# Kernel tuning notes

Measured on AMD Instinct MI355X. Metric: run time of the kernel, lower is better.

Reference implementation:

```python
import jax, jax.numpy as jnp
import numpy as np

EPS = 1e-5  # torch LayerNorm default

def _ln(x, w, b):
    mu = jnp.mean(x, axis=-1, keepdims=True)
    var = jnp.mean((x - mu) ** 2, axis=-1, keepdims=True)
    return (x - mu) * jax.lax.rsqrt(var + EPS) * w + b

def setup_inputs() -> dict:
    B, C, P, D = 256, 256, 256, 256  # broadcasting in final add requires B==P==C
    key = jax.random.key(0)
    ks = jax.random.split(key, 10)
    d_rsqrt = D ** -0.5
    return {
        "x": jax.random.normal(ks[0], (B, C), dtype=jnp.float32),
        "prev_cell_out": jax.random.normal(ks[1], (P, D), dtype=jnp.float32),
        "feature_emb_weight": jax.random.uniform(ks[2], (C, D), minval=-d_rsqrt, maxval=d_rsqrt),
        "feature_emb_bias": jax.random.uniform(ks[3], (1, C, D), minval=-d_rsqrt, maxval=d_rsqrt),
        "ln_emb_w": jnp.ones((D,), jnp.float32), "ln_emb_b": jnp.zeros((D,), jnp.float32),
        "ln_col_w": jnp.ones((D,), jnp.float32), "ln_col_b": jnp.zeros((D,), jnp.float32),
        "ln_prompt_w": jnp.ones((D,), jnp.float32), "ln_prompt_b": jnp.zeros((D,), jnp.float32),
        "dense_imp_w": jax.random.normal(ks[4], (D, 2 * D)) * (2 * D) ** -0.5,  # torch Linear weight [out,in]
        "dense_imp_b": jnp.zeros((D,), jnp.float32),
        "emb_column": jax.random.normal(ks[5], (C, D)) * 0.01,
        "emb_prompt": jax.random.normal(ks[6], (P, D)) * 0.01,
        "expand_weight": jax.random.normal(ks[7], (P, 1)),  # dense_expand.weight [n_prompts, 1]
        "expand_bias": jax.random.normal(ks[8], (P,)) * 0.01,
    }

def reference(x, prev_cell_out, feature_emb_weight, feature_emb_bias,
              ln_emb_w, ln_emb_b, ln_col_w, ln_col_b, ln_prompt_w, ln_prompt_b,
              dense_imp_w, dense_imp_b, emb_column, emb_prompt,
              expand_weight, expand_bias):
    # addcmul: bias + x[...,None] * weight -> [B, C, D]
    x_emb = _ln(jax.nn.relu(feature_emb_bias + x[..., None] * feature_emb_weight), ln_emb_w, ln_emb_b)
    # prompt path (unbatched): [P, 2D] -> [P, D]
    xp_in = jnp.concatenate([_ln(emb_prompt, ln_prompt_w, ln_prompt_b), prev_cell_out], axis=-1)
    x_prompt = xp_in @ dense_imp_w.T + dense_imp_b + emb_prompt
    x_col = _ln(emb_column, ln_col_w, ln_col_b)  # [C, D]
    mask = jax.nn.softmax(x_prompt @ x_col.T, axis=-1)  # [P, C]
    # einsum 'pc,bcd->bpd'
    x_out = jnp.einsum('pc,bcd->bpd', mask, x_emb)
    # 'pc,bcd,pa->bpd' with a==1 is the same contraction scaled per-prompt by expand_weight[p,0]
    x_out = x_out * (1.0 + expand_weight[:, 0])[None, :, None]
    # 'pc,p->pc' then unsqueeze(0).unsqueeze(-1): [1, P, C, 1]; broadcasts [B,P,D] -> [1,B,P,D]
    bias_term = (mask * expand_bias[:, None])[None, :, :, None]
    return x_out + bias_term  # [1, B, P, D] (B==P==C)
```

## Files before the change

### kernel.cpp

```cpp
#include <hip/hip_runtime.h>
#include <cstdint>

typedef _Float16 half8 __attribute__((ext_vector_type(8)));
typedef float f32x4 __attribute__((ext_vector_type(4)));

#define LN_EPS 1e-5f

__device__ __forceinline__ float dot4(float4 a, float4 b) {
  return a.x*b.x + a.y*b.y + a.z*b.z + a.w*b.w;
}

__global__ __launch_bounds__(256) void k_pre(
    const float* __restrict__ x, const float* __restrict__ few, const float* __restrict__ feb,
    const float* __restrict__ emb_pr, const float* __restrict__ lnp_w, const float* __restrict__ lnp_b,
    const float* __restrict__ prev, const float* __restrict__ W, const float* __restrict__ Wb,
    const float* __restrict__ emb_col, const float* __restrict__ lnc_w, const float* __restrict__ lnc_b,
    float2* __restrict__ stats2, float* __restrict__ mask_f32, _Float16* __restrict__ mask_f16)
{
  __shared__ __align__(16) struct {
    float xin[512];
    float xq[256];
    float sc[256];
    float wr1[4], wr2[4];
  } sm;

  int t = threadIdx.x, w = t >> 6, lane = t & 63;

  if (blockIdx.x >= 256) {
    int bid = blockIdx.x - 256;
    int b = bid >> 3;
    int cg = (bid & 7) * 4 + w;
    int c0 = cg * 8;
    float xv[8];
    #pragma unroll
    for (int j = 0; j < 8; ++j) xv[j] = x[b*256 + c0 + j];
    float s1[8], s2[8];
    #pragma unroll
    for (int j = 0; j < 8; ++j) { s1[j] = 0.f; s2[j] = 0.f; }
    #pragma unroll
    for (int j = 0; j < 8; ++j) {
      float4 fw = ((const float4*)few)[(c0+j)*64 + lane];
      float4 fb = ((const float4*)feb)[(c0+j)*64 + lane];
      float4 v;
      v.x = fmaxf(fb.x + xv[j]*fw.x, 0.f);
      v.y = fmaxf(fb.y + xv[j]*fw.y, 0.f);
      v.z = fmaxf(fb.z + xv[j]*fw.z, 0.f);
      v.w = fmaxf(fb.w + xv[j]*fw.w, 0.f);
      s1[j] += v.x + v.y + v.z + v.w;
      s2[j] += v.x*v.x + v.y*v.y + v.z*v.z + v.w*v.w;
    }
    #pragma unroll
    for (int o = 32; o > 0; o >>= 1) {
      #pragma unroll
      for (int j = 0; j < 8; ++j) { s1[j] += __shfl_xor(s1[j], o); s2[j] += __shfl_xor(s2[j], o); }
    }
    float mu[8], rs[8];
    #pragma unroll
    for (int j = 0; j < 8; ++j) {
      mu[j] = s1[j] * (1.0f/256.0f);
      float var = s2[j] * (1.0f/256.0f) - mu[j]*mu[j];
      rs[j] = rsqrtf(var + LN_EPS);
    }
    float muv = mu[0], rsv = rs[0];
    #pragma unroll
    for (int j = 1; j < 8; ++j) {
      muv = (lane == j) ? mu[j] : muv;
      rsv = (lane == j) ? rs[j] : rsv;
    }
    if (lane < 8) stats2[b*256 + c0 + lane] = make_float2(muv, rsv);
    return;
  }

  int p = blockIdx.x;
  int q = t & 3, g = t >> 2;

  {
    float4 v = ((const float4*)emb_pr)[p*64 + lane];
    float s1 = v.x + v.y + v.z + v.w;
    float s2 = v.x*v.x + v.y*v.y + v.z*v.z + v.w*v.w;
    #pragma unroll
    for (int o = 32; o > 0; o >>= 1) { s1 += __shfl_xor(s1, o); s2 += __shfl_xor(s2, o); }
    float mu = s1 * (1.0f/256.0f);
    float var = s2 * (1.0f/256.0f) - mu*mu;
    float rsv = rsqrtf(var + LN_EPS);
    float4 w4 = ((const float4*)lnp_w)[lane];
    float4 b4 = ((const float4*)lnp_b)[lane];
    float4 y;
    y.x = (v.x-mu)*rsv*w4.x + b4.x;  y.y = (v.y-mu)*rsv*w4.y + b4.y;
    y.z = (v.z-mu)*rsv*w4.z + b4.z;  y.w = (v.w-mu)*rsv*w4.w + b4.w;
    if (w == 0) {
      ((float4*)sm.xin)[lane] = y;
      ((float4*)sm.xin)[64 + lane] = ((const float4*)prev)[p*64 + lane];
    }
  }
  __syncthreads();

  {
    float acc[4] = {0.f, 0.f, 0.f, 0.f};
    #pragma unroll 4
    for (int j = 0; j < 32; ++j) {
      int k4 = j*4 + q;
      float4 xv = ((const float4*)sm.xin)[k4];
      #pragma unroll
      for (int pp = 0; pp < 4; ++pp) {
        int d = pp*64 + g;
        float4 wv = ((const float4*)W)[d*128 + k4];
        acc[pp] += dot4(wv, xv);
      }
    }
    #pragma unroll
    for (int pp = 0; pp < 4; ++pp) {
      acc[pp] += __shfl_xor(acc[pp], 1);
      acc[pp] += __shfl_xor(acc[pp], 2);
    }
    if (q == 0) {
      #pragma unroll
      for (int pp = 0; pp < 4; ++pp) {
        int d = pp*64 + g;
        sm.xq[d] = acc[pp] + Wb[d] + emb_pr[p*256 + d];
      }
    }
  }
  __syncthreads();

  {
    float s1[4] = {0,0,0,0}, s2[4] = {0,0,0,0};
    #pragma unroll 4
    for (int j = 0; j < 16; ++j) {
      int k4 = j*4 + q;
      #pragma unroll
      for (int pp = 0; pp < 4; ++pp) {
        float4 v = ((const float4*)emb_col)[(pp*64+g)*64 + k4];
        s1[pp] += v.x + v.y + v.z + v.w;
        s2[pp] += v.x*v.x + v.y*v.y + v.z*v.z + v.w*v.w;
      }
    }
    float mu[4], rs[4];
    #pragma unroll
    for (int pp = 0; pp < 4; ++pp) {
      s1[pp] += __shfl_xor(s1[pp], 1);  s1[pp] += __shfl_xor(s1[pp], 2);
      s2[pp] += __shfl_xor(s2[pp], 1);  s2[pp] += __shfl_xor(s2[pp], 2);
      mu[pp] = s1[pp] * (1.0f/256.0f);
      float var = s2[pp] * (1.0f/256.0f) - mu[pp]*mu[pp];
      rs[pp] = rsqrtf(var + LN_EPS);
    }
    float acc[4] = {0.f, 0.f, 0.f, 0.f};
    #pragma unroll 4
    for (int j = 0; j < 16; ++j) {
      int k4 = j*4 + q;
      float4 lw4 = ((const float4*)lnc_w)[k4];
      float4 lb4 = ((const float4*)lnc_b)[k4];
      float4 xv = ((const float4*)sm.xq)[k4];
      #pragma unroll
      for (int pp = 0; pp < 4; ++pp) {
        float4 v = ((const float4*)emb_col)[(pp*64+g)*64 + k4];
        float4 nc;
        nc.x = (v.x-mu[pp])*rs[pp]*lw4.x + lb4.x;
        nc.y = (v.y-mu[pp])*rs[pp]*lw4.y + lb4.y;
        nc.z = (v.z-mu[pp])*rs[pp]*lw4.z + lb4.z;
        nc.w = (v.w-mu[pp])*rs[pp]*lw4.w + lb4.w;
        acc[pp] += dot4(nc, xv);
      }
    }
    #pragma unroll
    for (int pp = 0; pp < 4; ++pp) {
      acc[pp] += __shfl_xor(acc[pp], 1);
      acc[pp] += __shfl_xor(acc[pp], 2);
    }
    if (q == 0) {
      #pragma unroll
      for (int pp = 0; pp < 4; ++pp) sm.sc[pp*64 + g] = acc[pp];
    }
  }
  __syncthreads();

  {
    float val = sm.sc[t];
    float m0 = val;
    #pragma unroll
    for (int o = 32; o > 0; o >>= 1) m0 = fmaxf(m0, __shfl_xor(m0, o));
    if (lane == 0) sm.wr1[w] = m0;
    __syncthreads();
    float M = fmaxf(fmaxf(sm.wr1[0], sm.wr1[1]), fmaxf(sm.wr1[2], sm.wr1[3]));
    float e = expf(val - M);
    float s = e;
    #pragma unroll
    for (int o = 32; o > 0; o >>= 1) s += __shfl_xor(s, o);
    if (lane == 0) sm.wr2[w] = s;
    __syncthreads();
    float S = sm.wr2[0] + sm.wr2[1] + sm.wr2[2] + sm.wr2[3];
    float mv = e / S;
    mask_f32[p*256 + t] = mv;
    mask_f16[p*256 + t] = (_Float16)mv;
  }
}

__global__ __launch_bounds__(256) void k_main(
    const float* __restrict__ x, const float* __restrict__ few, const float* __restrict__ feb,
    const float* __restrict__ ln_emb_w, const float* __restrict__ ln_emb_b,
    const float2* __restrict__ stats2,
    const _Float16* __restrict__ mask_f16, const float* __restrict__ mask_f32,
    const float* __restrict__ ew, const float* __restrict__ eb,
    float* __restrict__ out)
{
  __shared__ __align__(16) _Float16 Bs[2][8 * 64 * 8];
  __shared__ float xrow[256];
  __shared__ __align__(8) float2 srow[256];

  const int t = threadIdx.x, w = t >> 6, lane = t & 63;
  const int lm = lane & 15, quad = lane >> 4;
  const int b  = blockIdx.x >> 2;
  const int ds = (blockIdx.x & 3) * 64;
  const int dl = t & 63;
  const int d  = ds + dl;

  xrow[t] = x[b*256 + t];
  srow[t] = stats2[b*256 + t];
  const float lwv = ln_emb_w[d];
  const float lbv = ln_emb_b[d];

  f32x4 acc[4][4];
  #pragma unroll
  for (int i = 0; i < 4; ++i)
    #pragma unroll
    for (int j = 0; j < 4; ++j)
      acc[i][j] = (f32x4){0.f, 0.f, 0.f, 0.f};

  float fwv[16], fbv[16];
  #pragma unroll
  for (int j = 0; j < 16; ++j) {
    int cl = w*16 + j;
    fwv[j] = few[cl*256 + d];
    fbv[j] = feb[cl*256 + d];
  }
  __syncthreads();
  {
    half8 h0, h1;
    #pragma unroll
    for (int j = 0; j < 16; ++j) {
      int cl = w*16 + j;
      float2 st = srow[cl];
      float v = fmaxf(fbv[j] + xrow[cl]*fwv[j], 0.f);
      _Float16 hh = (_Float16)((v - st.x) * st.y * lwv + lbv);
      if (j < 8) h0[j] = hh; else h1[j-8] = hh;
    }
    *(half8*)(&Bs[0][((w*2 + 0)*64 + dl)*8]) = h0;
    *(half8*)(&Bs[0][((w*2 + 1)*64 + dl)*8]) = h1;
  }
  __syncthreads();

  for (int kb = 0; kb < 4; ++kb) {
    if (kb < 3) {
      #pragma unroll
      for (int j = 0; j < 16; ++j) {
        int cl = (kb+1)*64 + w*16 + j;
        fwv[j] = few[cl*256 + d];
        fbv[j] = feb[cl*256 + d];
      }
    }
    const _Float16* Bcur = &Bs[kb & 1][0];
    #pragma unroll
    for (int ks = 0; ks < 2; ++ks) {
      half8 af[4], bf[4];
      #pragma unroll
      for (int mt = 0; mt < 4; ++mt)
        af[mt] = *(const half8*)(mask_f16 + (size_t)(w*64 + mt*16 + lm)*256 + kb*64 + ks*32 + quad*8);
      #pragma unroll
      for (int nt = 0; nt < 4; ++nt)
        bf[nt] = *(const half8*)(Bcur + ((ks*4 + quad)*64 + nt*16 + lm)*8);
      #pragma unroll
      for (int mt = 0; mt < 4; ++mt)
        #pragma unroll
        for (int nt = 0; nt < 4; ++nt)
          acc[mt][nt] = __builtin_amdgcn_mfma_f32_16x16x32_f16(af[mt], bf[nt], acc[mt][nt], 0, 0, 0);
    }
    if (kb < 3) {
      half8 h0, h1;
      #pragma unroll
      for (int j = 0; j < 16; ++j) {
        int cl = (kb+1)*64 + w*16 + j;
        float2 st = srow[cl];
        float v = fmaxf(fbv[j] + xrow[cl]*fwv[j], 0.f);
        _Float16 hh = (_Float16)((v - st.x) * st.y * lwv + lbv);
        if (j < 8) h0[j] = hh; else h1[j-8] = hh;
      }
      *(half8*)(&Bs[(kb+1) & 1][((w*2 + 0)*64 + dl)*8]) = h0;
      *(half8*)(&Bs[(kb+1) & 1][((w*2 + 1)*64 + dl)*8]) = h1;
      __syncthreads();
    }
  }

  const float ebv = eb[b];
  #pragma unroll
  for (int mt = 0; mt < 4; ++mt) {
    float sp[4], tb[4];
    #pragma unroll
    for (int r = 0; r < 4; ++r) {
      int p = w*64 + mt*16 + quad*4 + r;
      sp[r] = 1.0f + ew[p];
      tb[r] = mask_f32[b*256 + p] * ebv;
    }
    #pragma unroll
    for (int nt = 0; nt < 4; ++nt) {
      int dd = ds + nt*16 + lm;
      #pragma unroll
      for (int r = 0; r < 4; ++r) {
        int p = w*64 + mt*16 + quad*4 + r;
        out[((size_t)b << 16) + ((size_t)p << 8) + dd] = acc[mt][nt][r] * sp[r] + tb[r];
      }
    }
  }
}

extern "C" void kernel_launch(void* const* d_in, const int* in_sizes, int n_in,
                              void* d_out, int out_size, void* d_ws, size_t ws_size,
                              hipStream_t stream) {
  const float* x        = (const float*)d_in[0];
  const float* prev     = (const float*)d_in[1];
  const float* few      = (const float*)d_in[2];
  const float* feb      = (const float*)d_in[3];
  const float* ln_emb_w = (const float*)d_in[4];
  const float* ln_emb_b = (const float*)d_in[5];
  const float* ln_col_w = (const float*)d_in[6];
  const float* ln_col_b = (const float*)d_in[7];
  const float* ln_pr_w  = (const float*)d_in[8];
  const float* ln_pr_b  = (const float*)d_in[9];
  const float* dimp_w   = (const float*)d_in[10];
  const float* dimp_b   = (const float*)d_in[11];
  const float* emb_col  = (const float*)d_in[12];
  const float* emb_pr   = (const float*)d_in[13];
  const float* ew       = (const float*)d_in[14];
  const float* eb       = (const float*)d_in[15];
  float* out = (float*)d_out;

  char* wsb = (char*)d_ws;
  float2*   ws_stats  = (float2*)(wsb);
  float*    ws_mask   = (float*)(wsb + 524288);
  _Float16* ws_mask_h = (_Float16*)(wsb + 786432);

  k_pre<<<dim3(256 + 2048), dim3(256), 0, stream>>>(
      x, few, feb,
      emb_pr, ln_pr_w, ln_pr_b, prev, dimp_w, dimp_b,
      emb_col, ln_col_w, ln_col_b,
      ws_stats, ws_mask, ws_mask_h);
  k_main<<<dim3(1024), dim3(256), 0, stream>>>(
      x, few, feb, ln_emb_w, ln_emb_b,
      ws_stats, ws_mask_h, ws_mask, ew, eb, out);
}
```

Measured before the change: 149.5 us.

## Swap MFMA operands for vectorized output stores and prefetch mask fragments

The MFMA operand roles are swapped so that the x_emb tile from LDS becomes the A operand and the mask the B operand. Each accumulator's four rows then run along d, so every lane writes its results with one 16-byte vector store instead of four scalar stores. Mask fragments for the next k-block are prefetched into registers during the current block's compute, and the kb loop is fully unrolled. This aims to cut store instruction count and hide global load latency, at the cost of higher register pressure.

```diff
diff --git a/kernel.cpp b/kernel.cpp
--- a/kernel.cpp
+++ b/kernel.cpp
@@ -214,6 +214,13 @@
   const int dl = t & 63;
   const int d  = ds + dl;
 
+  half8 mf[2][4];
+  #pragma unroll
+  for (int ks = 0; ks < 2; ++ks)
+    #pragma unroll
+    for (int nt = 0; nt < 4; ++nt)
+      mf[ks][nt] = *(const half8*)(mask_f16 + (size_t)(w*64 + nt*16 + lm)*256 + ks*32 + quad*8);
+
   xrow[t] = x[b*256 + t];
   srow[t] = stats2[b*256 + t];
   const float lwv = ln_emb_w[d];
@@ -249,6 +256,7 @@
   }
   __syncthreads();
 
+  #pragma unroll
   for (int kb = 0; kb < 4; ++kb) {
     if (kb < 3) {
       #pragma unroll
@@ -261,20 +269,22 @@
     const _Float16* Bcur = &Bs[kb & 1][0];
     #pragma unroll
     for (int ks = 0; ks < 2; ++ks) {
-      half8 af[4], bf[4];
+      half8 xf[4];
       #pragma unroll
       for (int mt = 0; mt < 4; ++mt)
-        af[mt] = *(const half8*)(mask_f16 + (size_t)(w*64 + mt*16 + lm)*256 + kb*64 + ks*32 + quad*8);
-      #pragma unroll
-      for (int nt = 0; nt < 4; ++nt)
-        bf[nt] = *(const half8*)(Bcur + ((ks*4 + quad)*64 + nt*16 + lm)*8);
+        xf[mt] = *(const half8*)(Bcur + ((ks*4 + quad)*64 + mt*16 + lm)*8);
       #pragma unroll
       for (int mt = 0; mt < 4; ++mt)
         #pragma unroll
         for (int nt = 0; nt < 4; ++nt)
-          acc[mt][nt] = __builtin_amdgcn_mfma_f32_16x16x32_f16(af[mt], bf[nt], acc[mt][nt], 0, 0, 0);
+          acc[mt][nt] = __builtin_amdgcn_mfma_f32_16x16x32_f16(xf[mt], mf[ks][nt], acc[mt][nt], 0, 0, 0);
     }
     if (kb < 3) {
+      #pragma unroll
+      for (int ks = 0; ks < 2; ++ks)
+        #pragma unroll
+        for (int nt = 0; nt < 4; ++nt)
+          mf[ks][nt] = *(const half8*)(mask_f16 + (size_t)(w*64 + nt*16 + lm)*256 + (kb+1)*64 + ks*32 + quad*8);
       half8 h0, h1;
       #pragma unroll
       for (int j = 0; j < 16; ++j) {
@@ -291,23 +301,21 @@
   }
 
   const float ebv = eb[b];
+  float sp[4], tb[4];
+  #pragma unroll
+  for (int nt = 0; nt < 4; ++nt) {
+    int p = w*64 + nt*16 + lm;
+    sp[nt] = 1.0f + ew[p];
+    tb[nt] = mask_f32[b*256 + p] * ebv;
+  }
   #pragma unroll
   for (int mt = 0; mt < 4; ++mt) {
-    float sp[4], tb[4];
-    #pragma unroll
-    for (int r = 0; r < 4; ++r) {
-      int p = w*64 + mt*16 + quad*4 + r;
-      sp[r] = 1.0f + ew[p];
-      tb[r] = mask_f32[b*256 + p] * ebv;
-    }
     #pragma unroll
     for (int nt = 0; nt < 4; ++nt) {
-      int dd = ds + nt*16 + lm;
-      #pragma unroll
-      for (int r = 0; r < 4; ++r) {
-        int p = w*64 + mt*16 + quad*4 + r;
-        out[((size_t)b << 16) + ((size_t)p << 8) + dd] = acc[mt][nt][r] * sp[r] + tb[r];
-      }
+      int p = w*64 + nt*16 + lm;
+      int dd = ds + mt*16 + quad*4;
+      f32x4 o = acc[mt][nt] * sp[nt] + tb[nt];
+      *(f32x4*)(out + ((size_t)b << 16) + ((size_t)p << 8) + dd) = o;
     }
   }
 }
```

New measurement: 148.1 us. No clear change (-1.0%).
